# Optimization experiments

Measured on AMD Instinct MI355X. Metric: run time of the kernel, lower is better.

The kernel has to match this reference:

```python
import jax, jax.numpy as jnp
import numpy as np

# Dims: lifted grid is N_X x N_Y, input signal has N_IN dims (= N_X*N_Y).
N_X, N_Y, N_IN = 32, 32, 1024
FILT = 33              # resolution-filter taps (odd, centered)
SIGMA0 = 0.1           # resolution_filter_initial_sigma (step 0 of decay schedule)
EPS = 1e-7


def _resolution_filter(sigma):
    # Gaussian taps on normalized coords in ~[-1, 1], normalized to sum 1.
    t = (jnp.arange(FILT, dtype=jnp.float32) - FILT // 2) * (2.0 / FILT)
    k = jnp.exp(-0.5 * jnp.square(t / sigma))
    return k / jnp.sum(k)


def _interpolate_lifting_map(lm_raw, filt):
    # Circular 1-D convolution of the generator parametrization with the
    # Gaussian resolution filter along the input-signal axis.
    P = N_X * N_Y
    pad = FILT // 2
    v = lm_raw.reshape(P, 1, N_IN)
    v = jnp.concatenate([v[..., -pad:], v, v[..., :pad]], axis=-1)  # wrap pad
    k = filt.reshape(1, 1, FILT)
    out = jax.lax.conv_general_dilated(
        v, k, window_strides=(1,), padding='VALID',
        dimension_numbers=('NCH', 'OIH', 'NCH'))
    return out.reshape(N_X, N_Y, N_IN)


def setup_inputs() -> dict:
    key = jax.random.key(0)
    k1, k2 = jax.random.split(key)
    x = jax.random.normal(k1, (16384, N_IN), dtype=jnp.float32)
    lm_raw = jax.random.normal(k2, (N_X, N_Y, N_IN), dtype=jnp.float32) / np.float32(np.sqrt(N_IN))
    return {"x": x, "lm_raw": lm_raw}


def reference(x, lm_raw):
    # _demean_and_normalize_input: per-sample demean + std-normalize.
    mu = jnp.mean(x, axis=-1, keepdims=True)
    sd = jnp.std(x, axis=-1, keepdims=True)
    xn = (x - mu) / (sd + EPS)
    # _sample_resolution_filter + _interpolate_lifting_map
    filt = _resolution_filter(jnp.asarray(SIGMA0, dtype=jnp.float32))
    lm = _interpolate_lifting_map(lm_raw, filt)  # [n_x, n_y, n_in]
    # _lift: y[b, i, j] = sum_n lm[i, j, n] * x[b, n]
    y = jnp.einsum('xyn,bn->bxy', lm, xn)
    return y
```

## Files before the change

kernel.cpp:

```cpp
#include <hip/hip_runtime.h>
#include <hip/hip_bf16.h>

#define N_IN   1024
#define N_P    1024
#define FILT   33
#define PAD    16

typedef __attribute__((ext_vector_type(8))) __bf16 bf16x8;
typedef __attribute__((ext_vector_type(4))) float  f32x4;

#define GLB(p) ((const __attribute__((address_space(1))) unsigned int*)(p))
#define LDSP(p) ((__attribute__((address_space(3))) unsigned int*)(p))

__device__ __forceinline__ unsigned short f2bf(float f) {
    union { __hip_bfloat16 h; unsigned short u; } cv;
    cv.h = __float2bfloat16(f);
    return cv.u;
}

__global__ __launch_bounds__(256)
void normalize_kernel(const float* __restrict__ x, __hip_bfloat16* __restrict__ xn)
{
    const int lane = threadIdx.x & 63;
    const int row  = blockIdx.x * 4 + (threadIdx.x >> 6);

    const float4* xr = reinterpret_cast<const float4*>(x + (size_t)row * N_IN);
    float4 v[4];
    float s = 0.f, s2 = 0.f;
#pragma unroll
    for (int i = 0; i < 4; i++) {
        v[i] = xr[i * 64 + lane];
        s  += v[i].x + v[i].y + v[i].z + v[i].w;
        s2 += v[i].x * v[i].x + v[i].y * v[i].y + v[i].z * v[i].z + v[i].w * v[i].w;
    }
#pragma unroll
    for (int off = 32; off > 0; off >>= 1) {
        s  += __shfl_xor(s,  off, 64);
        s2 += __shfl_xor(s2, off, 64);
    }
    const float mu  = s * (1.0f / N_IN);
    const float var = fmaxf(s2 * (1.0f / N_IN) - mu * mu, 0.0f);
    const float inv = 1.0f / (sqrtf(var) + 1e-7f);

    ushort4* outv = reinterpret_cast<ushort4*>(xn + (size_t)row * N_IN);
#pragma unroll
    for (int i = 0; i < 4; i++) {
        ushort4 o;
        o.x = f2bf((v[i].x - mu) * inv);
        o.y = f2bf((v[i].y - mu) * inv);
        o.z = f2bf((v[i].z - mu) * inv);
        o.w = f2bf((v[i].w - mu) * inv);
        outv[i * 64 + lane] = o;
    }
}

__global__ __launch_bounds__(256)
void conv_kernel(const float* __restrict__ lm_raw, __hip_bfloat16* __restrict__ lm)
{
    __shared__ float row[N_IN];
    __shared__ float fw[FILT];
    const int tid = threadIdx.x;
    const int p   = blockIdx.x;

    if (tid < FILT) {
        float t = (tid - PAD) * (2.0f / FILT);
        float u = t * 10.0f;
        fw[tid] = expf(-0.5f * u * u);
    }
    reinterpret_cast<float4*>(row)[tid] =
        reinterpret_cast<const float4*>(lm_raw + (size_t)p * N_IN)[tid];
    __syncthreads();

    float fsum = 0.f;
#pragma unroll
    for (int f = 0; f < FILT; f++) fsum += fw[f];
    const float inv = 1.0f / fsum;

    const int n0 = tid * 4;
    float o[4] = {0.f, 0.f, 0.f, 0.f};
#pragma unroll
    for (int f = 0; f < FILT; f++) {
        const float w = fw[f];
#pragma unroll
        for (int j = 0; j < 4; j++)
            o[j] += w * row[(n0 + j + f - PAD) & (N_IN - 1)];
    }
    ushort4 ov;
    ov.x = f2bf(o[0] * inv);
    ov.y = f2bf(o[1] * inv);
    ov.z = f2bf(o[2] * inv);
    ov.w = f2bf(o[3] * inv);
    reinterpret_cast<ushort4*>(lm + (size_t)p * N_IN)[tid] = ov;
}

__global__ __launch_bounds__(256, 2)
void gemm_bt(const __hip_bfloat16* __restrict__ A,
             const __hip_bfloat16* __restrict__ B,
             float* __restrict__ C,
             int M, int N, int K)
{
    constexpr int BM = 128, BN = 128, BK = 32;
    __shared__ __hip_bfloat16 As[BM * BK];
    __shared__ __hip_bfloat16 Bs[BN * BK];

    const int tid  = threadIdx.x;
    const int lane = tid & 63;
    const int wid  = tid >> 6;
    const int wr   = wid >> 1;
    const int wc   = wid & 1;

    const int bm = blockIdx.y * BM;
    const int bn = blockIdx.x * BN;

    const int srow = lane >> 2;
    const int scol = (lane & 3) * 8;
    const __hip_bfloat16* gA0 = A + (size_t)(bm + wid * 32 + srow) * K + scol;
    const __hip_bfloat16* gA1 = gA0 + (size_t)16 * K;
    const __hip_bfloat16* gB0 = B + (size_t)(bn + wid * 32 + srow) * K + scol;
    const __hip_bfloat16* gB1 = gB0 + (size_t)16 * K;
    __hip_bfloat16* lA0 = As + (wid * 32) * BK;
    __hip_bfloat16* lA1 = As + (wid * 32 + 16) * BK;
    __hip_bfloat16* lB0 = Bs + (wid * 32) * BK;
    __hip_bfloat16* lB1 = Bs + (wid * 32 + 16) * BK;

    f32x4 acc[4][4] = {};

    const bf16x8* Asv = reinterpret_cast<const bf16x8*>(As);
    const bf16x8* Bsv = reinterpret_cast<const bf16x8*>(Bs);
    const int lr = lane & 15;
    const int kb = lane >> 4;

    for (int k0 = 0; k0 < K; k0 += BK) {
        __builtin_amdgcn_global_load_lds(GLB(gA0 + k0), LDSP(lA0), 16, 0, 0);
        __builtin_amdgcn_global_load_lds(GLB(gA1 + k0), LDSP(lA1), 16, 0, 0);
        __builtin_amdgcn_global_load_lds(GLB(gB0 + k0), LDSP(lB0), 16, 0, 0);
        __builtin_amdgcn_global_load_lds(GLB(gB1 + k0), LDSP(lB1), 16, 0, 0);
        __syncthreads();

        bf16x8 a[4], b[4];
#pragma unroll
        for (int m = 0; m < 4; m++) a[m] = Asv[(wr * 64 + m * 16 + lr) * 4 + kb];
#pragma unroll
        for (int n = 0; n < 4; n++) b[n] = Bsv[(wc * 64 + n * 16 + lr) * 4 + kb];
#pragma unroll
        for (int m = 0; m < 4; m++)
#pragma unroll
            for (int n = 0; n < 4; n++)
                acc[m][n] = __builtin_amdgcn_mfma_f32_16x16x32_bf16(a[m], b[n], acc[m][n], 0, 0, 0);
        __syncthreads();
    }

    const int crow0 = (lane >> 4) * 4;
    const int ccol  = lane & 15;
#pragma unroll
    for (int m = 0; m < 4; m++)
#pragma unroll
        for (int n = 0; n < 4; n++) {
#pragma unroll
            for (int r = 0; r < 4; r++) {
                const int row = bm + wr * 64 + m * 16 + crow0 + r;
                const int col = bn + wc * 64 + n * 16 + ccol;
                C[(size_t)row * N + col] = acc[m][n][r];
            }
        }
}

extern "C" void kernel_launch(void* const* d_in, const int* in_sizes, int n_in,
                              void* d_out, int out_size, void* d_ws, size_t ws_size,
                              hipStream_t stream) {
    const float* x      = (const float*)d_in[0];
    const float* lm_raw = (const float*)d_in[1];
    float* out = (float*)d_out;

    const int M = in_sizes[0] / N_IN;

    __hip_bfloat16* xn = (__hip_bfloat16*)d_ws;
    __hip_bfloat16* lm = (__hip_bfloat16*)((char*)d_ws + (size_t)M * N_IN * 2);

    normalize_kernel<<<M / 4, 256, 0, stream>>>(x, xn);
    conv_kernel<<<N_P, 256, 0, stream>>>(lm_raw, lm);

    dim3 grid(N_P / 128, M / 128);
    gemm_bt<<<grid, dim3(256), 0, stream>>>(xn, lm, out, M, N_P, N_IN);
}
```

Baseline: 76.99 us.

## Rewrite GEMM with 256x256 tiles, 4-stage LDS pipeline, swizzle and XCD remap

New measurement: 65.58 us. -14.8%, faster.

```diff
diff --git a/kernel.cpp b/kernel.cpp
--- a/kernel.cpp
+++ b/kernel.cpp
@@ -93,74 +93,97 @@
     reinterpret_cast<ushort4*>(lm + (size_t)p * N_IN)[tid] = ov;
 }
 
-__global__ __launch_bounds__(256, 2)
-void gemm_bt(const __hip_bfloat16* __restrict__ A,
-             const __hip_bfloat16* __restrict__ B,
-             float* __restrict__ C,
-             int M, int N, int K)
+__global__ __launch_bounds__(512, 2)
+void gemm_bt2(const __hip_bfloat16* __restrict__ A,
+              const __hip_bfloat16* __restrict__ B,
+              float* __restrict__ C,
+              int M, int N, int K)
 {
-    constexpr int BM = 128, BN = 128, BK = 32;
-    __shared__ __hip_bfloat16 As[BM * BK];
-    __shared__ __hip_bfloat16 Bs[BN * BK];
-
-    const int tid  = threadIdx.x;
-    const int lane = tid & 63;
-    const int wid  = tid >> 6;
-    const int wr   = wid >> 1;
-    const int wc   = wid & 1;
-
-    const int bm = blockIdx.y * BM;
-    const int bn = blockIdx.x * BN;
-
-    const int srow = lane >> 2;
-    const int scol = (lane & 3) * 8;
-    const __hip_bfloat16* gA0 = A + (size_t)(bm + wid * 32 + srow) * K + scol;
-    const __hip_bfloat16* gA1 = gA0 + (size_t)16 * K;
-    const __hip_bfloat16* gB0 = B + (size_t)(bn + wid * 32 + srow) * K + scol;
-    const __hip_bfloat16* gB1 = gB0 + (size_t)16 * K;
-    __hip_bfloat16* lA0 = As + (wid * 32) * BK;
-    __hip_bfloat16* lA1 = As + (wid * 32 + 16) * BK;
-    __hip_bfloat16* lB0 = Bs + (wid * 32) * BK;
-    __hip_bfloat16* lB1 = Bs + (wid * 32 + 16) * BK;
-
-    f32x4 acc[4][4] = {};
-
-    const bf16x8* Asv = reinterpret_cast<const bf16x8*>(As);
-    const bf16x8* Bsv = reinterpret_cast<const bf16x8*>(Bs);
-    const int lr = lane & 15;
-    const int kb = lane >> 4;
-
-    for (int k0 = 0; k0 < K; k0 += BK) {
-        __builtin_amdgcn_global_load_lds(GLB(gA0 + k0), LDSP(lA0), 16, 0, 0);
-        __builtin_amdgcn_global_load_lds(GLB(gA1 + k0), LDSP(lA1), 16, 0, 0);
-        __builtin_amdgcn_global_load_lds(GLB(gB0 + k0), LDSP(lB0), 16, 0, 0);
-        __builtin_amdgcn_global_load_lds(GLB(gB1 + k0), LDSP(lB1), 16, 0, 0);
-        __syncthreads();
-
-        bf16x8 a[4], b[4];
-#pragma unroll
-        for (int m = 0; m < 4; m++) a[m] = Asv[(wr * 64 + m * 16 + lr) * 4 + kb];
-#pragma unroll
-        for (int n = 0; n < 4; n++) b[n] = Bsv[(wc * 64 + n * 16 + lr) * 4 + kb];
-#pragma unroll
-        for (int m = 0; m < 4; m++)
+    constexpr int BK = 32;
+    __shared__ char smem[4][32768];
+
+    const int tid = threadIdx.x;
+    const int l   = tid & 63;
+    const int w   = tid >> 6;
+    const int wr  = w >> 2;
+    const int wc  = w & 3;
+
+    const int o    = blockIdx.x;
+    const int lin  = (o & 7) * (gridDim.x >> 3) + (o >> 3);
+    const int tn   = lin & 3;
+    const int tm   = lin >> 2;
+    const size_t bm = (size_t)tm * 256;
+    const size_t bn = (size_t)tn * 256;
+
+    const int srow = w * 16 + (l >> 2);
+    const int scol = 16 * ((l & 3) ^ ((l >> 3) & 3));
+    const char* gA = (const char*)(A + (bm + srow) * (size_t)K) + scol;
+    const char* gB = (const char*)(B + (bn + srow) * (size_t)K) + scol;
+    const size_t rowstep = (size_t)128 * K * 2;
+
+#define STAGE(t, b) do {                                                        \
+    const char* a0_ = gA + (size_t)(t) * (BK * 2);                              \
+    const char* b0_ = gB + (size_t)(t) * (BK * 2);                              \
+    char* La_ = &smem[(b)][0]     + w * 1024;                                   \
+    char* Lb_ = &smem[(b)][16384] + w * 1024;                                   \
+    __builtin_amdgcn_global_load_lds(GLB(a0_),           LDSP(La_),        16, 0, 0); \
+    __builtin_amdgcn_global_load_lds(GLB(a0_ + rowstep), LDSP(La_ + 8192), 16, 0, 0); \
+    __builtin_amdgcn_global_load_lds(GLB(b0_),           LDSP(Lb_),        16, 0, 0); \
+    __builtin_amdgcn_global_load_lds(GLB(b0_ + rowstep), LDSP(Lb_ + 8192), 16, 0, 0); \
+} while (0)
+
+    const int lr = l & 15;
+    const int kb = l >> 4;
+    const int rslot = 16 * (kb ^ ((lr >> 1) & 3));
+
+    f32x4 acc[8][4] = {};
+
+    const int NT = K / BK;
+
+    STAGE(0, 0);
+    STAGE(1, 1);
+    STAGE(2, 2);
+
+    for (int t = 0; t < NT; ++t) {
+        asm volatile("s_waitcnt lgkmcnt(0)" ::: "memory");
+        if (t < NT - 2)       asm volatile("s_waitcnt vmcnt(8)" ::: "memory");
+        else if (t == NT - 2) asm volatile("s_waitcnt vmcnt(4)" ::: "memory");
+        else                  asm volatile("s_waitcnt vmcnt(0)" ::: "memory");
+        __builtin_amdgcn_s_barrier();
+        asm volatile("" ::: "memory");
+
+        if (t + 3 < NT) STAGE(t + 3, (t + 3) & 3);
+
+        const char* Ab = &smem[t & 3][0];
+        const char* Bb = &smem[t & 3][16384];
+
+        bf16x8 bfr[4], afr[8];
+#pragma unroll
+        for (int n = 0; n < 4; n++)
+            bfr[n] = *(const bf16x8*)(Bb + (wc * 64 + n * 16 + lr) * 64 + rslot);
+#pragma unroll
+        for (int m = 0; m < 8; m++)
+            afr[m] = *(const bf16x8*)(Ab + (wr * 128 + m * 16 + lr) * 64 + rslot);
+
+#pragma unroll
+        for (int m = 0; m < 8; m++)
 #pragma unroll
             for (int n = 0; n < 4; n++)
-                acc[m][n] = __builtin_amdgcn_mfma_f32_16x16x32_bf16(a[m], b[n], acc[m][n], 0, 0, 0);
-        __syncthreads();
-    }
-
-    const int crow0 = (lane >> 4) * 4;
-    const int ccol  = lane & 15;
-#pragma unroll
-    for (int m = 0; m < 4; m++)
+                acc[m][n] = __builtin_amdgcn_mfma_f32_16x16x32_bf16(afr[m], bfr[n], acc[m][n], 0, 0, 0);
+    }
+#undef STAGE
+
+    const int crow = (l >> 4) * 4;
+    const int ccol = l & 15;
+#pragma unroll
+    for (int m = 0; m < 8; m++)
 #pragma unroll
         for (int n = 0; n < 4; n++) {
 #pragma unroll
             for (int r = 0; r < 4; r++) {
-                const int row = bm + wr * 64 + m * 16 + crow0 + r;
-                const int col = bn + wc * 64 + n * 16 + ccol;
-                C[(size_t)row * N + col] = acc[m][n][r];
+                const size_t row = bm + wr * 128 + m * 16 + crow + r;
+                const size_t col = bn + wc * 64 + n * 16 + ccol;
+                C[row * N + col] = acc[m][n][r];
             }
         }
 }
@@ -180,6 +203,6 @@
     normalize_kernel<<<M / 4, 256, 0, stream>>>(x, xn);
     conv_kernel<<<N_P, 256, 0, stream>>>(lm_raw, lm);
 
-    dim3 grid(N_P / 128, M / 128);
-    gemm_bt<<<grid, dim3(256), 0, stream>>>(xn, lm, out, M, N_P, N_IN);
-}
+    const int nblk = (M / 256) * (N_P / 256);
+    gemm_bt2<<<nblk, dim3(512), 0, stream>>>(xn, lm, out, M, N_P, N_IN);
+}
```
